# Optimization experiments

Measured on AMD Instinct MI355X. Metric: run time of the kernel, lower is better.

The kernel has to match this reference:

```python
import jax, jax.numpy as jnp
import numpy as np

NEG_SLOPE = 0.2  # PyG GATv2Conv default


def _glorot(key, shape):
    fan_in, fan_out = shape[0], shape[1]
    lim = (6.0 / (fan_in + fan_out)) ** 0.5
    return jax.random.uniform(key, shape, jnp.float32, -lim, lim)


def setup_inputs() -> dict:
    key = jax.random.key(0)
    ks = jax.random.split(key, 20)
    N, E = 30000, 480000
    IN, HID, H, OUT = 16, 64, 4, 2
    d1 = HID * H  # 256
    inp = {
        "x": jax.random.normal(ks[0], (N, IN), jnp.float32),
        "edge_index": jax.random.randint(ks[1], (2, E), 0, N, jnp.int64),
        # conv1: in=16 -> heads=4, out=64, concat
        "Wl1": _glorot(ks[2], (IN, d1)), "bl1": jnp.zeros((d1,), jnp.float32),
        "Wr1": _glorot(ks[3], (IN, d1)), "br1": jnp.zeros((d1,), jnp.float32),
        "att1": _glorot(ks[4], (H, HID)), "b1": jnp.zeros((d1,), jnp.float32),
        # conv2: 256 -> heads=4, out=64, concat
        "Wl2": _glorot(ks[5], (d1, d1)), "bl2": jnp.zeros((d1,), jnp.float32),
        "Wr2": _glorot(ks[6], (d1, d1)), "br2": jnp.zeros((d1,), jnp.float32),
        "att2": _glorot(ks[7], (H, HID)), "b2": jnp.zeros((d1,), jnp.float32),
        # conv3: 256 -> heads=1, out=64, mean (concat=False)
        "Wl3": _glorot(ks[8], (d1, HID)), "bl3": jnp.zeros((HID,), jnp.float32),
        "Wr3": _glorot(ks[9], (d1, HID)), "br3": jnp.zeros((HID,), jnp.float32),
        "att3": _glorot(ks[10], (1, HID)), "b3": jnp.zeros((HID,), jnp.float32),
        # fc: 64 -> 2
        "Wfc": _glorot(ks[11], (HID, OUT)), "bfc": jnp.zeros((OUT,), jnp.float32),
    }
    return inp


def _gatv2(x, Wl, bl, Wr, br, att, b, src, dst, n_nodes, concat):
    """One GATv2Conv layer (PyG semantics, share_weights=False, eval mode)."""
    H, C = att.shape
    xl = (x @ Wl + bl).reshape(-1, H, C)  # source projection [N,H,C]
    xr = (x @ Wr + br).reshape(-1, H, C)  # target projection [N,H,C]
    # per-edge attention logit: a^T leaky_relu(xl_j + xr_i)
    e = jax.nn.leaky_relu(xl[src] + xr[dst], NEG_SLOPE)          # [E,H,C]
    score = jnp.einsum('ehc,hc->eh', e, att)                     # [E,H]
    # segment softmax over edges sharing the same destination node
    m = jax.ops.segment_max(score, dst, num_segments=n_nodes)    # [N,H]
    p = jnp.exp(score - m[dst])
    s = jax.ops.segment_sum(p, dst, num_segments=n_nodes)        # [N,H]
    alpha = p / (s[dst] + 1e-16)                                 # [E,H]
    out = jax.ops.segment_sum(alpha[:, :, None] * xl[src], dst,
                              num_segments=n_nodes)              # [N,H,C]
    out = out.reshape(n_nodes, H * C) if concat else out.mean(axis=1)
    return out + b


def reference(x, edge_index, Wl1, bl1, Wr1, br1, att1, b1,
              Wl2, bl2, Wr2, br2, att2, b2,
              Wl3, bl3, Wr3, br3, att3, b3, Wfc, bfc):
    n = x.shape[0]
    # PyG GATv2Conv adds self-loops by default
    loops = jnp.arange(n, dtype=edge_index.dtype)
    src = jnp.concatenate([edge_index[0], loops])
    dst = jnp.concatenate([edge_index[1], loops])
    # dropout(p=0.6) is identity in eval mode
    h = jax.nn.elu(_gatv2(x, Wl1, bl1, Wr1, br1, att1, b1, src, dst, n, True))
    h = jax.nn.elu(_gatv2(h, Wl2, bl2, Wr2, br2, att2, b2, src, dst, n, True))
    h = _gatv2(h, Wl3, bl3, Wr3, br3, att3, b3, src, dst, n, False)
    return h @ Wfc + bfc
```

## Files before the change

kernel.cpp:

```cpp
#include <hip/hip_runtime.h>
#include <math.h>

typedef __attribute__((ext_vector_type(8))) short bf16x8;
typedef __attribute__((ext_vector_type(4))) float f32x4;
typedef __attribute__((ext_vector_type(2))) float f32x2;

__device__ inline unsigned short f2bf(float f) {
    union { float f; unsigned u; } v; v.f = f;
    unsigned r = v.u + 0x7FFFu + ((v.u >> 16) & 1u);
    return (unsigned short)(r >> 16);
}
__device__ inline float bf2f(unsigned short s) {
    union { unsigned u; float f; } v; v.u = ((unsigned)s) << 16;
    return v.f;
}

__device__ inline void wconv_elem(const float* __restrict__ W,
                                  unsigned short* __restrict__ Bh,
                                  unsigned short* __restrict__ Bl,
                                  int idx, int NC) {
    int k = idx / NC, n = idx - k * NC;
    float f = W[idx];
    unsigned short h = f2bf(f);
    Bh[n * 256 + k] = h;
    Bl[n * 256 + k] = f2bf(f - bf2f(h));
}

__global__ __launch_bounds__(256) void k_prep(int* __restrict__ deg, int N,
                                              const float* __restrict__ Wl2,
                                              const float* __restrict__ Wr2,
                                              const float* __restrict__ Wl3,
                                              const float* __restrict__ Wr3,
                                              unsigned short* __restrict__ W2lh,
                                              unsigned short* __restrict__ W2ll,
                                              unsigned short* __restrict__ W2rh,
                                              unsigned short* __restrict__ W2rl,
                                              unsigned short* __restrict__ W3lh,
                                              unsigned short* __restrict__ W3ll,
                                              unsigned short* __restrict__ W3rh,
                                              unsigned short* __restrict__ W3rl) {
    int idx = blockIdx.x * 256 + threadIdx.x;
    if (idx < N) { deg[idx] = 1; return; }
    idx -= N;
    if (idx < 65536) { wconv_elem(Wl2, W2lh, W2ll, idx, 256); return; }
    idx -= 65536;
    if (idx < 65536) { wconv_elem(Wr2, W2rh, W2rl, idx, 256); return; }
    idx -= 65536;
    if (idx < 16384) { wconv_elem(Wl3, W3lh, W3ll, idx, 64); return; }
    idx -= 16384;
    if (idx < 16384) { wconv_elem(Wr3, W3rh, W3rl, idx, 64); }
}

__global__ __launch_bounds__(256) void k_count(const int* __restrict__ dst, int E,
                                               int* __restrict__ deg) {
    int e = blockIdx.x * 256 + threadIdx.x;
    if (e < E) atomicAdd(&deg[dst[e]], 1);
}

__global__ __launch_bounds__(1024) void k_scan1(const int* __restrict__ deg,
                                                int* __restrict__ excl,
                                                int* __restrict__ bsum, int N) {
    __shared__ int wsum[17];
    int t = threadIdx.x, lane = t & 63, wid = t >> 6;
    int idx = blockIdx.x * 1024 + t;
    int v = (idx < N) ? deg[idx] : 0;
    int x = v;
    #pragma unroll
    for (int off = 1; off < 64; off <<= 1) {
        int y = __shfl_up(x, off, 64);
        if (lane >= off) x += y;
    }
    if (lane == 63) wsum[wid] = x;
    __syncthreads();
    if (wid == 0 && lane < 16) {
        int w = wsum[lane];
        int xs = w;
        #pragma unroll
        for (int off = 1; off < 16; off <<= 1) {
            int y = __shfl_up(xs, off, 64);
            if (lane >= off) xs += y;
        }
        wsum[lane] = xs - w;
        if (lane == 15) wsum[16] = xs;
    }
    __syncthreads();
    int incl = x + wsum[wid];
    if (idx < N) excl[idx] = incl - v;
    if (t == 0) bsum[blockIdx.x] = wsum[16];
}

__global__ __launch_bounds__(1024) void k_scan23(const int* __restrict__ excl,
                                                 const int* __restrict__ bsum,
                                                 int* __restrict__ rowptr,
                                                 int* __restrict__ cursor, int N, int nb) {
    __shared__ int s_off, s_tot;
    int t = threadIdx.x;
    if (t < 64) {
        int v = (t < nb) ? bsum[t] : 0;
        int x = v;
        #pragma unroll
        for (int off = 1; off < 64; off <<= 1) {
            int y = __shfl_up(x, off, 64);
            if (t >= off) x += y;
        }
        if (t == (int)blockIdx.x) s_off = x - v;
        if (t == 63) s_tot = x;
    }
    __syncthreads();
    int idx = blockIdx.x * 1024 + t;
    if (idx < N) {
        int e = excl[idx] + s_off;
        rowptr[idx] = e;
        cursor[idx] = e;
    }
    if (idx == 0) rowptr[N] = s_tot;
}

__global__ __launch_bounds__(256) void k_scatter(const int* __restrict__ src,
                                                 const int* __restrict__ dst,
                                                 int E, int N,
                                                 int* __restrict__ cursor,
                                                 int* __restrict__ col) {
    int idx = blockIdx.x * 256 + threadIdx.x;
    if (idx < E) {
        int d = dst[idx];
        int pos = atomicAdd(&cursor[d], 1);
        col[pos] = src[idx];
    } else if (idx < E + N) {
        int i = idx - E;
        int pos = atomicAdd(&cursor[i], 1);
        col[pos] = i;
    }
}

__global__ __launch_bounds__(256) void gemm_bias2(const float* __restrict__ A,
                                                  const float* __restrict__ W1,
                                                  const float* __restrict__ b1,
                                                  const float* __restrict__ W2,
                                                  const float* __restrict__ b2,
                                                  unsigned short* __restrict__ C1b,
                                                  float* __restrict__ C2,
                                                  int M, int K, int NC) {
    __shared__ float As[16][68];
    __shared__ float Bs[2][16][68];
    int tid = threadIdx.x;
    int tx = tid & 15, ty = tid >> 4;
    int m0 = blockIdx.x * 64, n0 = blockIdx.y * 64;
    float acc[2][4][4] = {};
    for (int k0 = 0; k0 < K; k0 += 16) {
        #pragma unroll
        for (int i = 0; i < 4; ++i) {
            int idx = tid + i * 256;
            int r = idx >> 4, c = idx & 15;
            int row = m0 + r;
            As[c][r] = (row < M) ? A[(size_t)row * K + k0 + c] : 0.f;
        }
        #pragma unroll
        for (int i = 0; i < 4; ++i) {
            int idx = tid + i * 256;
            int r = idx >> 6, c = idx & 63;
            Bs[0][r][c] = W1[(size_t)(k0 + r) * NC + n0 + c];
            Bs[1][r][c] = W2[(size_t)(k0 + r) * NC + n0 + c];
        }
        __syncthreads();
        #pragma unroll
        for (int k = 0; k < 16; ++k) {
            float a[4], b[4], b2v[4];
            #pragma unroll
            for (int i = 0; i < 4; ++i) a[i] = As[k][ty * 4 + i];
            #pragma unroll
            for (int i = 0; i < 4; ++i) b[i] = Bs[0][k][tx * 4 + i];
            #pragma unroll
            for (int i = 0; i < 4; ++i) b2v[i] = Bs[1][k][tx * 4 + i];
            #pragma unroll
            for (int i = 0; i < 4; ++i)
                #pragma unroll
                for (int j = 0; j < 4; ++j) {
                    acc[0][i][j] += a[i] * b[j];
                    acc[1][i][j] += a[i] * b2v[j];
                }
        }
        __syncthreads();
    }
    #pragma unroll
    for (int i = 0; i < 4; ++i) {
        int row = m0 + ty * 4 + i;
        if (row < M) {
            #pragma unroll
            for (int j = 0; j < 4; ++j) {
                int cn = n0 + tx * 4 + j;
                C1b[(size_t)row * NC + cn] = f2bf(acc[0][i][j] + b1[cn]);
                C2[(size_t)row * NC + cn] = acc[1][i][j] + b2[cn];
            }
        }
    }
}

#define LDA 40

template<int NF>
__global__ __launch_bounds__(512) void gemm_dual(const unsigned short* __restrict__ Ahg,
                                                 const unsigned short* __restrict__ Alg,
                                                 const unsigned short* __restrict__ B1hg,
                                                 const unsigned short* __restrict__ B1lg,
                                                 const unsigned short* __restrict__ B2hg,
                                                 const unsigned short* __restrict__ B2lg,
                                                 const float* __restrict__ bias1,
                                                 const float* __restrict__ bias2,
                                                 unsigned short* __restrict__ C1b,
                                                 float* __restrict__ C2,
                                                 int M, int NC) {
    const int KD = 256;
    const int BN = NF * 64;
    __shared__ unsigned short Ah[128 * LDA], Al[128 * LDA];
    __shared__ unsigned short Bs[4][BN * LDA];

    int tid = threadIdx.x;
    int lane = tid & 63;
    int wid = tid >> 6;
    int m0 = blockIdx.x * 128;
    int n0 = blockIdx.y * BN;
    int wm = (wid >> 2) * 64;
    int wn = (wid & 3) * (NF * 16);
    int r16 = lane & 15;
    int g8 = (lane >> 4) * 8;
    int g = lane >> 4;

    int srow = tid >> 2;
    int schunk = (tid & 3) * 8;
    int arow_g = m0 + srow;
    if (arow_g >= M) arow_g = M - 1;
    const unsigned short* gAh = Ahg + (size_t)arow_g * KD + schunk;
    const unsigned short* gAl = Alg + (size_t)arow_g * KD + schunk;
    bool bact = (NF == 2) || (tid < 256);
    int bcol = (NF == 2) ? srow : (tid >> 2);
    size_t boff = (size_t)(n0 + (bcol < BN ? bcol : 0)) * KD + schunk;
    const unsigned short* gB[4] = { B1hg + boff, B1lg + boff, B2hg + boff, B2lg + boff };

    f32x4 acc[2][4][NF];
    #pragma unroll
    for (int o = 0; o < 2; ++o)
        #pragma unroll
        for (int mf = 0; mf < 4; ++mf)
            #pragma unroll
            for (int nf = 0; nf < NF; ++nf)
                #pragma unroll
                for (int q = 0; q < 4; ++q) acc[o][mf][nf][q] = 0.f;

    bf16x8 sa_h = *(const bf16x8*)gAh;
    bf16x8 sa_l = *(const bf16x8*)gAl;
    bf16x8 sb0, sb1, sb2, sb3;
    if (bact) {
        sb0 = *(const bf16x8*)gB[0];
        sb1 = *(const bf16x8*)gB[1];
        sb2 = *(const bf16x8*)gB[2];
        sb3 = *(const bf16x8*)gB[3];
    }

    for (int k = 0; k < 8; ++k) {
        __syncthreads();
        *(bf16x8*)&Ah[srow * LDA + schunk] = sa_h;
        *(bf16x8*)&Al[srow * LDA + schunk] = sa_l;
        if (bact) {
            *(bf16x8*)&Bs[0][bcol * LDA + schunk] = sb0;
            *(bf16x8*)&Bs[1][bcol * LDA + schunk] = sb1;
            *(bf16x8*)&Bs[2][bcol * LDA + schunk] = sb2;
            *(bf16x8*)&Bs[3][bcol * LDA + schunk] = sb3;
        }
        __syncthreads();
        if (k < 7) {
            int k0n = (k + 1) * 32;
            sa_h = *(const bf16x8*)(gAh + k0n);
            sa_l = *(const bf16x8*)(gAl + k0n);
            if (bact) {
                sb0 = *(const bf16x8*)(gB[0] + k0n);
                sb1 = *(const bf16x8*)(gB[1] + k0n);
                sb2 = *(const bf16x8*)(gB[2] + k0n);
                sb3 = *(const bf16x8*)(gB[3] + k0n);
            }
        }
        bf16x8 ah[4], al[4];
        #pragma unroll
        for (int mf = 0; mf < 4; ++mf) {
            int base = (wm + mf * 16 + r16) * LDA + g8;
            ah[mf] = *(const bf16x8*)&Ah[base];
            al[mf] = *(const bf16x8*)&Al[base];
        }
        #pragma unroll
        for (int o = 0; o < 2; ++o) {
            #pragma unroll
            for (int nf = 0; nf < NF; ++nf) {
                int base = (wn + nf * 16 + r16) * LDA + g8;
                bf16x8 bh = *(const bf16x8*)&Bs[o * 2 + 0][base];
                bf16x8 bl = *(const bf16x8*)&Bs[o * 2 + 1][base];
                #pragma unroll
                for (int mf = 0; mf < 4; ++mf) {
                    acc[o][mf][nf] = __builtin_amdgcn_mfma_f32_16x16x32_bf16(ah[mf], bh, acc[o][mf][nf], 0, 0, 0);
                    acc[o][mf][nf] = __builtin_amdgcn_mfma_f32_16x16x32_bf16(ah[mf], bl, acc[o][mf][nf], 0, 0, 0);
                    acc[o][mf][nf] = __builtin_amdgcn_mfma_f32_16x16x32_bf16(al[mf], bh, acc[o][mf][nf], 0, 0, 0);
                }
            }
        }
    }

    #pragma unroll
    for (int nf = 0; nf < NF; ++nf) {
        int cn = n0 + wn + nf * 16 + r16;
        float bv1 = bias1[cn], bv2 = bias2[cn];
        #pragma unroll
        for (int mf = 0; mf < 4; ++mf) {
            #pragma unroll
            for (int r = 0; r < 4; ++r) {
                int row = m0 + wm + mf * 16 + g * 4 + r;
                if (row < M) {
                    C1b[(size_t)row * NC + cn] = f2bf(acc[0][mf][nf][r] + bv1);
                    C2[(size_t)row * NC + cn] = acc[1][mf][nf][r] + bv2;
                }
            }
        }
    }
}

__global__ __launch_bounds__(128) void gat_agg4(const unsigned short* __restrict__ xlb,
                                                const float* __restrict__ xr,
                                                const float* __restrict__ att,
                                                const float* __restrict__ bias,
                                                const int* __restrict__ rowptr,
                                                const int* __restrict__ col,
                                                unsigned short* __restrict__ Hh,
                                                unsigned short* __restrict__ Hl,
                                                int N) {
    int i = blockIdx.x * 2 + (threadIdx.x >> 6);
    int lane = threadIdx.x & 63;
    if (i >= N) return;
    int sub = lane & 31;
    int half = lane >> 5;
    const float L2E = 1.44269504089f;
    f32x2 xr2[4], a06[4], a04[4];
    {
        float4 a = *(const float4*)(xr + (size_t)i * 256 + sub * 8);
        float4 b = *(const float4*)(xr + (size_t)i * 256 + sub * 8 + 4);
        xr2[0].x = a.x; xr2[0].y = a.y; xr2[1].x = a.z; xr2[1].y = a.w;
        xr2[2].x = b.x; xr2[2].y = b.y; xr2[3].x = b.z; xr2[3].y = b.w;
        float4 c = *(const float4*)(att + sub * 8);
        float4 d = *(const float4*)(att + sub * 8 + 4);
        float av[8] = {c.x, c.y, c.z, c.w, d.x, d.y, d.z, d.w};
        #pragma unroll
        for (int q = 0; q < 4; ++q) {
            a06[q].x = av[2 * q] * (0.6f * L2E);     a06[q].y = av[2 * q + 1] * (0.6f * L2E);
            a04[q].x = av[2 * q] * (0.4f * L2E);     a04[q].y = av[2 * q + 1] * (0.4f * L2E);
        }
    }
    int e0 = rowptr[i], e1 = rowptr[i + 1];
    int nE = e1 - e0;
    int T = (nE + 1) >> 1;

    auto jl = [&](int t) -> int {
        int idx = 2 * t + half;
        idx = idx < nE ? idx : nE - 1;
        return col[e0 + idx];
    };
    auto ld = [&](int j) -> bf16x8 {
        return *(const bf16x8*)(xlb + (size_t)j * 256 + sub * 8);
    };

    float ss = 0.f;
    f32x2 acc2[4] = {};

    #define PROC(R, IT) { \
        union { bf16x8 v; unsigned u[4]; } uu; uu.v = (R); \
        f32x2 va_[4]; \
        f32x2 s06_ = {0.f, 0.f}, s04_ = {0.f, 0.f}; \
        _Pragma("unroll") \
        for (int q = 0; q < 4; ++q) { \
            union { unsigned a; float f; } lo_, hi_; \
            lo_.a = uu.u[q] << 16; hi_.a = uu.u[q] & 0xffff0000u; \
            va_[q].x = lo_.f; va_[q].y = hi_.f; \
            f32x2 t_ = va_[q] + xr2[q]; \
            s06_ += t_ * a06[q]; \
            f32x2 ab_; \
            ab_.x = __builtin_fabsf(t_.x); ab_.y = __builtin_fabsf(t_.y); \
            s04_ += ab_ * a04[q]; \
        } \
        f32x2 sc_ = s06_ + s04_; \
        float s_ = sc_.x + sc_.y; \
        s_ += __shfl_xor(s_, 1); \
        s_ += __shfl_xor(s_, 2); \
        s_ += __shfl_xor(s_, 4); \
        bool valid_ = (2 * (IT) + half) < nE; \
        float p_ = valid_ ? __builtin_amdgcn_exp2f(s_) : 0.f; \
        ss += p_; \
        f32x2 pp_; pp_.x = p_; pp_.y = p_; \
        _Pragma("unroll") \
        for (int q = 0; q < 4; ++q) acc2[q] += pp_ * va_[q]; \
    }

    int j0 = jl(0), j1 = jl(1), j2 = jl(2), j3 = jl(3);
    bf16x8 r0 = ld(j0), r1 = ld(j1), r2 = ld(j2), r3 = ld(j3);
    int j4 = jl(4), j5 = jl(5), j6 = jl(6), j7 = jl(7);
    bf16x8 r4 = ld(j4), r5 = ld(j5), r6 = ld(j6), r7 = ld(j7);
    j0 = jl(8); j1 = jl(9); j2 = jl(10); j3 = jl(11);

    int t = 0;
    while (t + 8 <= T) {
        PROC(r0, t + 0); PROC(r1, t + 1); PROC(r2, t + 2); PROC(r3, t + 3);
        r0 = ld(j0); r1 = ld(j1); r2 = ld(j2); r3 = ld(j3);
        j0 = jl(t + 12); j1 = jl(t + 13); j2 = jl(t + 14); j3 = jl(t + 15);
        PROC(r4, t + 4); PROC(r5, t + 5); PROC(r6, t + 6); PROC(r7, t + 7);
        r4 = ld(j0); r5 = ld(j1); r6 = ld(j2); r7 = ld(j3);
        j0 = jl(t + 16); j1 = jl(t + 17); j2 = jl(t + 18); j3 = jl(t + 19);
        t += 8;
    }
    if (t + 0 < T) PROC(r0, t + 0);
    if (t + 1 < T) PROC(r1, t + 1);
    if (t + 2 < T) PROC(r2, t + 2);
    if (t + 3 < T) PROC(r3, t + 3);
    if (t + 4 < T) PROC(r4, t + 4);
    if (t + 5 < T) PROC(r5, t + 5);
    if (t + 6 < T) PROC(r6, t + 6);
    if (t + 7 < T) PROC(r7, t + 7);
    #undef PROC

    ss += __shfl_xor(ss, 32);
    #pragma unroll
    for (int q = 0; q < 4; ++q) {
        acc2[q].x += __shfl_xor(acc2[q].x, 32);
        acc2[q].y += __shfl_xor(acc2[q].y, 32);
    }

    if (lane < 32) {
        float inv = 1.f / ss;
        float accf[8];
        #pragma unroll
        for (int q = 0; q < 4; ++q) { accf[2 * q] = acc2[q].x; accf[2 * q + 1] = acc2[q].y; }
        bf16x8 hv, lv;
        #pragma unroll
        for (int c = 0; c < 8; ++c) {
            float o = fmaf(accf[c], inv, bias[sub * 8 + c]);
            o = o > 0.f ? o : __expf(o) - 1.f;
            unsigned short h_ = f2bf(o);
            hv[c] = (short)h_;
            lv[c] = (short)f2bf(o - bf2f(h_));
        }
        *(bf16x8*)(Hh + (size_t)i * 256 + sub * 8) = hv;
        *(bf16x8*)(Hl + (size_t)i * 256 + sub * 8) = lv;
    }
}

__global__ __launch_bounds__(128) void gat_agg1_fc(const unsigned short* __restrict__ xlb,
                                                   const float* __restrict__ xr,
                                                   const float* __restrict__ att,
                                                   const float* __restrict__ bias,
                                                   const float* __restrict__ Wfc,
                                                   const float* __restrict__ bfc,
                                                   const int* __restrict__ rowptr,
                                                   const int* __restrict__ col,
                                                   float* __restrict__ out, int N) {
    int i = blockIdx.x * 2 + (threadIdx.x >> 6);
    int lane = threadIdx.x & 63;
    if (i >= N) return;
    int sub = lane & 15;
    int qh = lane >> 4;
    const float L2E = 1.44269504089f;
    f32x2 xr2[2], a06[2], a04[2];
    {
        float4 a = *(const float4*)(xr + (size_t)i * 64 + sub * 4);
        xr2[0].x = a.x; xr2[0].y = a.y; xr2[1].x = a.z; xr2[1].y = a.w;
        float4 c = *(const float4*)(att + sub * 4);
        float av[4] = {c.x, c.y, c.z, c.w};
        #pragma unroll
        for (int q = 0; q < 2; ++q) {
            a06[q].x = av[2 * q] * (0.6f * L2E);     a06[q].y = av[2 * q + 1] * (0.6f * L2E);
            a04[q].x = av[2 * q] * (0.4f * L2E);     a04[q].y = av[2 * q + 1] * (0.4f * L2E);
        }
    }
    int e0 = rowptr[i], e1 = rowptr[i + 1];
    int nE = e1 - e0;
    int T = (nE + 3) >> 2;

    auto jl = [&](int t) -> int {
        int idx = 4 * t + qh;
        idx = idx < nE ? idx : nE - 1;
        return col[e0 + idx];
    };
    auto ld = [&](int j) -> ushort4 {
        return *(const ushort4*)(xlb + (size_t)j * 64 + sub * 4);
    };

    float ss = 0.f;
    f32x2 acc2[2] = {};

    #define PROC1(R, IT) { \
        ushort4 rr_ = (R); \
        f32x2 va_[2]; \
        { union { unsigned a; float f; } c0_, c1_, c2_, c3_; \
          c0_.a = ((unsigned)rr_.x) << 16; c1_.a = ((unsigned)rr_.y) << 16; \
          c2_.a = ((unsigned)rr_.z) << 16; c3_.a = ((unsigned)rr_.w) << 16; \
          va_[0].x = c0_.f; va_[0].y = c1_.f; va_[1].x = c2_.f; va_[1].y = c3_.f; } \
        f32x2 s06_ = {0.f, 0.f}, s04_ = {0.f, 0.f}; \
        _Pragma("unroll") \
        for (int q = 0; q < 2; ++q) { \
            f32x2 t_ = va_[q] + xr2[q]; \
            s06_ += t_ * a06[q]; \
            f32x2 ab_; \
            ab_.x = __builtin_fabsf(t_.x); ab_.y = __builtin_fabsf(t_.y); \
            s04_ += ab_ * a04[q]; \
        } \
        f32x2 sc_ = s06_ + s04_; \
        float s_ = sc_.x + sc_.y; \
        s_ += __shfl_xor(s_, 1); \
        s_ += __shfl_xor(s_, 2); \
        s_ += __shfl_xor(s_, 4); \
        s_ += __shfl_xor(s_, 8); \
        bool valid_ = (4 * (IT) + qh) < nE; \
        float p_ = valid_ ? __builtin_amdgcn_exp2f(s_) : 0.f; \
        ss += p_; \
        f32x2 pp_; pp_.x = p_; pp_.y = p_; \
        acc2[0] += pp_ * va_[0]; \
        acc2[1] += pp_ * va_[1]; \
    }

    int j0 = jl(0), j1 = jl(1), j2 = jl(2), j3 = jl(3);
    ushort4 r0 = ld(j0), r1 = ld(j1), r2 = ld(j2), r3 = ld(j3);
    int j4 = jl(4), j5 = jl(5), j6 = jl(6), j7 = jl(7);
    ushort4 r4 = ld(j4), r5 = ld(j5), r6 = ld(j6), r7 = ld(j7);
    j0 = jl(8); j1 = jl(9); j2 = jl(10); j3 = jl(11);

    int t = 0;
    while (t + 8 <= T) {
        PROC1(r0, t + 0); PROC1(r1, t + 1); PROC1(r2, t + 2); PROC1(r3, t + 3);
        r0 = ld(j0); r1 = ld(j1); r2 = ld(j2); r3 = ld(j3);
        j0 = jl(t + 12); j1 = jl(t + 13); j2 = jl(t + 14); j3 = jl(t + 15);
        PROC1(r4, t + 4); PROC1(r5, t + 5); PROC1(r6, t + 6); PROC1(r7, t + 7);
        r4 = ld(j0); r5 = ld(j1); r6 = ld(j2); r7 = ld(j3);
        j0 = jl(t + 16); j1 = jl(t + 17); j2 = jl(t + 18); j3 = jl(t + 19);
        t += 8;
    }
    if (t + 0 < T) PROC1(r0, t + 0);
    if (t + 1 < T) PROC1(r1, t + 1);
    if (t + 2 < T) PROC1(r2, t + 2);
    if (t + 3 < T) PROC1(r3, t + 3);
    if (t + 4 < T) PROC1(r4, t + 4);
    if (t + 5 < T) PROC1(r5, t + 5);
    if (t + 6 < T) PROC1(r6, t + 6);
    if (t + 7 < T) PROC1(r7, t + 7);
    #undef PROC1

    ss += __shfl_xor(ss, 16);
    ss += __shfl_xor(ss, 32);
    float accf[4] = {acc2[0].x, acc2[0].y, acc2[1].x, acc2[1].y};
    #pragma unroll
    for (int c = 0; c < 4; ++c) {
        accf[c] += __shfl_xor(accf[c], 16);
        accf[c] += __shfl_xor(accf[c], 32);
    }

    float inv = 1.f / ss;
    float q0 = 0.f, q1 = 0.f;
    #pragma unroll
    for (int c = 0; c < 4; ++c) {
        float h = fmaf(accf[c], inv, bias[sub * 4 + c]);
        q0 = fmaf(h, Wfc[(sub * 4 + c) * 2 + 0], q0);
        q1 = fmaf(h, Wfc[(sub * 4 + c) * 2 + 1], q1);
    }
    q0 += __shfl_xor(q0, 1); q1 += __shfl_xor(q1, 1);
    q0 += __shfl_xor(q0, 2); q1 += __shfl_xor(q1, 2);
    q0 += __shfl_xor(q0, 4); q1 += __shfl_xor(q1, 4);
    q0 += __shfl_xor(q0, 8); q1 += __shfl_xor(q1, 8);
    if (lane == 0) {
        out[(size_t)i * 2 + 0] = q0 + bfc[0];
        out[(size_t)i * 2 + 1] = q1 + bfc[1];
    }
}

extern "C" void kernel_launch(void* const* d_in, const int* in_sizes, int n_in,
                              void* d_out, int out_size, void* d_ws, size_t ws_size,
                              hipStream_t stream) {
    const float* x    = (const float*)d_in[0];
    const int*   ei   = (const int*)d_in[1];
    const float* Wl1  = (const float*)d_in[2];
    const float* bl1  = (const float*)d_in[3];
    const float* Wr1  = (const float*)d_in[4];
    const float* br1  = (const float*)d_in[5];
    const float* att1 = (const float*)d_in[6];
    const float* b1   = (const float*)d_in[7];
    const float* Wl2  = (const float*)d_in[8];
    const float* bl2  = (const float*)d_in[9];
    const float* Wr2  = (const float*)d_in[10];
    const float* br2  = (const float*)d_in[11];
    const float* att2 = (const float*)d_in[12];
    const float* b2   = (const float*)d_in[13];
    const float* Wl3  = (const float*)d_in[14];
    const float* bl3  = (const float*)d_in[15];
    const float* Wr3  = (const float*)d_in[16];
    const float* br3  = (const float*)d_in[17];
    const float* att3 = (const float*)d_in[18];
    const float* b3   = (const float*)d_in[19];
    const float* Wfc  = (const float*)d_in[20];
    const float* bfc  = (const float*)d_in[21];
    float* out = (float*)d_out;

    const int N = in_sizes[0] / 16;
    const int E = in_sizes[1] / 2;
    const int* srcp = ei;
    const int* dstp = ei + E;

    char* ws = (char*)d_ws;
    size_t off = 0;
    auto take = [&](size_t bytes) -> char* {
        char* p = ws + off;
        off = (off + bytes + 255) & ~(size_t)255;
        return p;
    };
    const int nb = (N + 1023) / 1024;
    int* rowptr = (int*)take((size_t)(N + 1) * 4);
    int* cursor = (int*)take((size_t)N * 4);
    int* deg    = (int*)take((size_t)N * 4);
    int* excl   = (int*)take((size_t)N * 4);
    int* bsum   = (int*)take((size_t)(nb + 1) * 4);
    int* col    = (int*)take((size_t)(E + N) * 4);
    unsigned short* xlb = (unsigned short*)take((size_t)N * 256 * 2);
    float* xr   = (float*)take((size_t)N * 256 * 4);
    unsigned short* Hh = (unsigned short*)take((size_t)N * 256 * 2);
    unsigned short* Hl = (unsigned short*)take((size_t)N * 256 * 2);
    unsigned short* W2lh = (unsigned short*)take(256 * 256 * 2);
    unsigned short* W2ll = (unsigned short*)take(256 * 256 * 2);
    unsigned short* W2rh = (unsigned short*)take(256 * 256 * 2);
    unsigned short* W2rl = (unsigned short*)take(256 * 256 * 2);
    unsigned short* W3lh = (unsigned short*)take(256 * 64 * 2);
    unsigned short* W3ll = (unsigned short*)take(256 * 64 * 2);
    unsigned short* W3rh = (unsigned short*)take(256 * 64 * 2);
    unsigned short* W3rl = (unsigned short*)take(256 * 64 * 2);
    (void)ws_size; (void)n_in; (void)out_size;

    {
        int total = N + 65536 + 65536 + 16384 + 16384;
        k_prep<<<dim3((total + 255) / 256), dim3(256), 0, stream>>>(
            deg, N, Wl2, Wr2, Wl3, Wr3,
            W2lh, W2ll, W2rh, W2rl, W3lh, W3ll, W3rh, W3rl);
    }
    k_count<<<dim3((E + 255) / 256), dim3(256), 0, stream>>>(dstp, E, deg);
    k_scan1<<<dim3(nb), dim3(1024), 0, stream>>>(deg, excl, bsum, N);
    k_scan23<<<dim3(nb), dim3(1024), 0, stream>>>(excl, bsum, rowptr, cursor, N, nb);
    k_scatter<<<dim3((E + N + 255) / 256), dim3(256), 0, stream>>>(srcp, dstp, E, N, cursor, col);

    dim3 agg_grid((N + 1) / 2);
    int mblk = (N + 127) / 128;

    gemm_bias2<<<dim3((N + 63) / 64, 4), dim3(256), 0, stream>>>(
        x, Wl1, bl1, Wr1, br1, xlb, xr, N, 16, 256);
    gat_agg4<<<agg_grid, dim3(128), 0, stream>>>(xlb, xr, att1, b1, rowptr, col, Hh, Hl, N);

    gemm_dual<2><<<dim3(mblk, 2), dim3(512), 0, stream>>>(
        Hh, Hl, W2lh, W2ll, W2rh, W2rl, bl2, br2, xlb, xr, N, 256);
    gat_agg4<<<agg_grid, dim3(128), 0, stream>>>(xlb, xr, att2, b2, rowptr, col, Hh, Hl, N);

    gemm_dual<1><<<dim3(mblk, 1), dim3(512), 0, stream>>>(
        Hh, Hl, W3lh, W3ll, W3rh, W3rl, bl3, br3, xlb, xr, N, 64);
    gat_agg1_fc<<<agg_grid, dim3(128), 0, stream>>>(xlb, xr, att3, b3, Wfc, bfc, rowptr, col, out, N);
}
```

Measured before the change: 253.8 us.

## Use contiguous edge halves per sub-wave, one node per block, swap GEMM grid axes

```diff
diff --git a/kernel.cpp b/kernel.cpp
--- a/kernel.cpp
+++ b/kernel.cpp
@@ -130,6 +130,8 @@
         int i = idx - E;
         int pos = atomicAdd(&cursor[i], 1);
         col[pos] = i;
+    } else if (idx < E + N + 64) {
+        col[idx] = 0;
     }
 }
 
@@ -145,7 +147,7 @@
     __shared__ float Bs[2][16][68];
     int tid = threadIdx.x;
     int tx = tid & 15, ty = tid >> 4;
-    int m0 = blockIdx.x * 64, n0 = blockIdx.y * 64;
+    int m0 = blockIdx.y * 64, n0 = blockIdx.x * 64;
     float acc[2][4][4] = {};
     for (int k0 = 0; k0 < K; k0 += 16) {
         #pragma unroll
@@ -218,8 +220,8 @@
     int tid = threadIdx.x;
     int lane = tid & 63;
     int wid = tid >> 6;
-    int m0 = blockIdx.x * 128;
-    int n0 = blockIdx.y * BN;
+    int m0 = blockIdx.y * 128;
+    int n0 = blockIdx.x * BN;
     int wm = (wid >> 2) * 64;
     int wn = (wid & 3) * (NF * 16);
     int r16 = lane & 15;
@@ -321,18 +323,17 @@
     }
 }
 
-__global__ __launch_bounds__(128) void gat_agg4(const unsigned short* __restrict__ xlb,
-                                                const float* __restrict__ xr,
-                                                const float* __restrict__ att,
-                                                const float* __restrict__ bias,
-                                                const int* __restrict__ rowptr,
-                                                const int* __restrict__ col,
-                                                unsigned short* __restrict__ Hh,
-                                                unsigned short* __restrict__ Hl,
-                                                int N) {
-    int i = blockIdx.x * 2 + (threadIdx.x >> 6);
-    int lane = threadIdx.x & 63;
-    if (i >= N) return;
+__global__ __launch_bounds__(64) void gat_agg4(const unsigned short* __restrict__ xlb,
+                                               const float* __restrict__ xr,
+                                               const float* __restrict__ att,
+                                               const float* __restrict__ bias,
+                                               const int* __restrict__ rowptr,
+                                               const int* __restrict__ col,
+                                               unsigned short* __restrict__ Hh,
+                                               unsigned short* __restrict__ Hl,
+                                               int N) {
+    int i = blockIdx.x;
+    int lane = threadIdx.x;
     int sub = lane & 31;
     int half = lane >> 5;
     const float L2E = 1.44269504089f;
@@ -354,12 +355,11 @@
     int e0 = rowptr[i], e1 = rowptr[i + 1];
     int nE = e1 - e0;
     int T = (nE + 1) >> 1;
-
-    auto jl = [&](int t) -> int {
-        int idx = 2 * t + half;
-        idx = idx < nE ? idx : nE - 1;
-        return col[e0 + idx];
-    };
+    int lim = half ? (nE - T) : T;
+    int limL = lim > 0 ? lim - 1 : 0;
+    const int* cb = col + e0 + (half ? T : 0);
+
+    auto jl = [&](int t) -> int { return cb[t < limL ? t : limL]; };
     auto ld = [&](int j) -> bf16x8 {
         return *(const bf16x8*)(xlb + (size_t)j * 256 + sub * 8);
     };
@@ -387,7 +387,7 @@
         s_ += __shfl_xor(s_, 1); \
         s_ += __shfl_xor(s_, 2); \
         s_ += __shfl_xor(s_, 4); \
-        bool valid_ = (2 * (IT) + half) < nE; \
+        bool valid_ = (IT) < lim; \
         float p_ = valid_ ? __builtin_amdgcn_exp2f(s_) : 0.f; \
         ss += p_; \
         f32x2 pp_; pp_.x = p_; pp_.y = p_; \
@@ -447,18 +447,17 @@
     }
 }
 
-__global__ __launch_bounds__(128) void gat_agg1_fc(const unsigned short* __restrict__ xlb,
-                                                   const float* __restrict__ xr,
-                                                   const float* __restrict__ att,
-                                                   const float* __restrict__ bias,
-                                                   const float* __restrict__ Wfc,
-                                                   const float* __restrict__ bfc,
-                                                   const int* __restrict__ rowptr,
-                                                   const int* __restrict__ col,
-                                                   float* __restrict__ out, int N) {
-    int i = blockIdx.x * 2 + (threadIdx.x >> 6);
-    int lane = threadIdx.x & 63;
-    if (i >= N) return;
+__global__ __launch_bounds__(64) void gat_agg1_fc(const unsigned short* __restrict__ xlb,
+                                                  const float* __restrict__ xr,
+                                                  const float* __restrict__ att,
+                                                  const float* __restrict__ bias,
+                                                  const float* __restrict__ Wfc,
+                                                  const float* __restrict__ bfc,
+                                                  const int* __restrict__ rowptr,
+                                                  const int* __restrict__ col,
+                                                  float* __restrict__ out, int N) {
+    int i = blockIdx.x;
+    int lane = threadIdx.x;
     int sub = lane & 15;
     int qh = lane >> 4;
     const float L2E = 1.44269504089f;
@@ -477,12 +476,12 @@
     int e0 = rowptr[i], e1 = rowptr[i + 1];
     int nE = e1 - e0;
     int T = (nE + 3) >> 2;
-
-    auto jl = [&](int t) -> int {
-        int idx = 4 * t + qh;
-        idx = idx < nE ? idx : nE - 1;
-        return col[e0 + idx];
-    };
+    int lim = nE - qh * T;
+    lim = lim < 0 ? 0 : (lim > T ? T : lim);
+    int limL = lim > 0 ? lim - 1 : 0;
+    const int* cb = col + e0 + qh * T;
+
+    auto jl = [&](int t) -> int { return cb[t < limL ? t : limL]; };
     auto ld = [&](int j) -> ushort4 {
         return *(const ushort4*)(xlb + (size_t)j * 64 + sub * 4);
     };
@@ -512,7 +511,7 @@
         s_ += __shfl_xor(s_, 2); \
         s_ += __shfl_xor(s_, 4); \
         s_ += __shfl_xor(s_, 8); \
-        bool valid_ = (4 * (IT) + qh) < nE; \
+        bool valid_ = (IT) < lim; \
         float p_ = valid_ ? __builtin_amdgcn_exp2f(s_) : 0.f; \
         ss += p_; \
         f32x2 pp_; pp_.x = p_; pp_.y = p_; \
@@ -618,7 +617,7 @@
     int* deg    = (int*)take((size_t)N * 4);
     int* excl   = (int*)take((size_t)N * 4);
     int* bsum   = (int*)take((size_t)(nb + 1) * 4);
-    int* col    = (int*)take((size_t)(E + N) * 4);
+    int* col    = (int*)take((size_t)(E + N + 64) * 4);
     unsigned short* xlb = (unsigned short*)take((size_t)N * 256 * 2);
     float* xr   = (float*)take((size_t)N * 256 * 4);
     unsigned short* Hh = (unsigned short*)take((size_t)N * 256 * 2);
@@ -642,20 +641,20 @@
     k_count<<<dim3((E + 255) / 256), dim3(256), 0, stream>>>(dstp, E, deg);
     k_scan1<<<dim3(nb), dim3(1024), 0, stream>>>(deg, excl, bsum, N);
     k_scan23<<<dim3(nb), dim3(1024), 0, stream>>>(excl, bsum, rowptr, cursor, N, nb);
-    k_scatter<<<dim3((E + N + 255) / 256), dim3(256), 0, stream>>>(srcp, dstp, E, N, cursor, col);
-
-    dim3 agg_grid((N + 1) / 2);
+    k_scatter<<<dim3((E + N + 64 + 255) / 256), dim3(256), 0, stream>>>(srcp, dstp, E, N, cursor, col);
+
+    dim3 agg_grid(N);
     int mblk = (N + 127) / 128;
 
-    gemm_bias2<<<dim3((N + 63) / 64, 4), dim3(256), 0, stream>>>(
+    gemm_bias2<<<dim3(4, (N + 63) / 64), dim3(256), 0, stream>>>(
         x, Wl1, bl1, Wr1, br1, xlb, xr, N, 16, 256);
-    gat_agg4<<<agg_grid, dim3(128), 0, stream>>>(xlb, xr, att1, b1, rowptr, col, Hh, Hl, N);
-
-    gemm_dual<2><<<dim3(mblk, 2), dim3(512), 0, stream>>>(
+    gat_agg4<<<agg_grid, dim3(64), 0, stream>>>(xlb, xr, att1, b1, rowptr, col, Hh, Hl, N);
+
+    gemm_dual<2><<<dim3(2, mblk), dim3(512), 0, stream>>>(
         Hh, Hl, W2lh, W2ll, W2rh, W2rl, bl2, br2, xlb, xr, N, 256);
-    gat_agg4<<<agg_grid, dim3(128), 0, stream>>>(xlb, xr, att2, b2, rowptr, col, Hh, Hl, N);
-
-    gemm_dual<1><<<dim3(mblk, 1), dim3(512), 0, stream>>>(
+    gat_agg4<<<agg_grid, dim3(64), 0, stream>>>(xlb, xr, att2, b2, rowptr, col, Hh, Hl, N);
+
+    gemm_dual<1><<<dim3(1, mblk), dim3(512), 0, stream>>>(
         Hh, Hl, W3lh, W3ll, W3rh, W3rl, bl3, br3, xlb, xr, N, 64);
-    gat_agg1_fc<<<agg_grid, dim3(128), 0, stream>>>(xlb, xr, att3, b3, Wfc, bfc, rowptr, col, out, N);
-}
+    gat_agg1_fc<<<agg_grid, dim3(64), 0, stream>>>(xlb, xr, att3, b3, Wfc, bfc, rowptr, col, out, N);
+}
```

Result: faster. 242.9 us (-4.3%).
